# Kernel tuning notes

Hardware: AMD Instinct MI355X
Metric: run time of the kernel (lower is better)

The kernel has to match this reference:

```python
import jax, jax.numpy as jnp
import numpy as np

THETA = 10000.0

def _rope(x, pos):
    # x: [b, h, s, hd]; pos: [s]
    hd = x.shape[-1]
    inv_freq = 1.0 / (THETA ** (jnp.arange(0, hd, 2, dtype=jnp.float32) / hd))  # [hd/2]
    ang = pos.astype(jnp.float32)[:, None] * inv_freq[None, :]                   # [s, hd/2]
    cos, sin = jnp.cos(ang), jnp.sin(ang)
    x1, x2 = x[..., 0::2], x[..., 1::2]
    r1 = x1 * cos - x2 * sin
    r2 = x1 * sin + x2 * cos
    return jnp.stack([r1, r2], axis=-1).reshape(x.shape)

def setup_inputs() -> dict:
    key = jax.random.key(0)
    ks = jax.random.split(key, 5)
    b, s, d = 2, 2048, 1024
    scale = 0.02
    return {
        "x": jax.random.normal(ks[0], (b, s, d), dtype=jnp.float32),
        "Wq": jax.random.normal(ks[1], (d, d), dtype=jnp.float32) * scale,
        "Wk": jax.random.normal(ks[2], (d, d), dtype=jnp.float32) * scale,
        "Wv": jax.random.normal(ks[3], (d, d), dtype=jnp.float32) * scale,
        "Wo": jax.random.normal(ks[4], (d, d), dtype=jnp.float32) * scale,
    }

def reference(x, Wq, Wk, Wv, Wo):
    b, s, d = x.shape
    n_heads = 16
    hd = d // n_heads

    def split_heads(t):  # [b,s,d] -> [b,h,s,hd]
        return t.reshape(b, s, n_heads, hd).transpose(0, 2, 1, 3)

    q = split_heads(x @ Wq.T)
    k = split_heads(x @ Wk.T)
    v = split_heads(x @ Wv.T)

    pos = jnp.arange(s)
    q = _rope(q, pos)
    k = _rope(k, pos)

    scores = jnp.einsum("bhqd,bhkd->bhqk", q, k) / jnp.sqrt(jnp.float32(hd))
    causal = jnp.tril(jnp.ones((s, s), dtype=bool))
    scores = jnp.where(causal, scores, -jnp.inf)
    attn = jax.nn.softmax(scores, axis=-1)
    ctx = jnp.einsum("bhqk,bhkd->bhqd", attn, v)
    ctx = ctx.transpose(0, 2, 1, 3).reshape(b, s, d)
    return ctx @ Wo.T
```

## Files before the change

kernel.cpp:

```cpp
#include <hip/hip_runtime.h>
#include <math.h>

#define B  2
#define S  2048
#define D  1024
#define NH 16
#define HD 64
#define NROWS (B * S)

#define AS1 __attribute__((address_space(1)))
#define AS3 __attribute__((address_space(3)))
#define GLD16(g, l) __builtin_amdgcn_global_load_lds((const AS1 void*)(g), (AS3 void*)(l), 16, 0, 0)

typedef __attribute__((ext_vector_type(8))) short short8;
typedef __attribute__((ext_vector_type(4))) float floatx4;

#define MFMA16(a, b, c) __builtin_amdgcn_mfma_f32_16x16x32_bf16((a), (b), (c), 0, 0, 0)

__device__ inline float fexp2(float x) { return __builtin_amdgcn_exp2f(x); }

__device__ inline unsigned short f2bf(float f) {
    union { float f; unsigned int u; } v; v.f = f;
    unsigned int u = v.u;
    u += 0x7fffu + ((u >> 16) & 1);
    return (unsigned short)(u >> 16);
}

__device__ inline unsigned int pack2bf(float a, float b) {
    unsigned int ua = __float_as_uint(a) + 0x8000u;
    unsigned int ub = __float_as_uint(b) + 0x8000u;
    return __builtin_amdgcn_perm(ub, ua, 0x07060302u);
}

__global__ __launch_bounds__(256) void cvt_kernel(
    const float* __restrict__ x,  const float* __restrict__ Wq,
    const float* __restrict__ Wk, const float* __restrict__ Wv,
    const float* __restrict__ Wo,
    unsigned short* __restrict__ xb,  unsigned short* __restrict__ wqb,
    unsigned short* __restrict__ wkb, unsigned short* __restrict__ wvb,
    unsigned short* __restrict__ wob, float2* __restrict__ tab)
{
    size_t idx = (size_t)blockIdx.x * 256 + threadIdx.x;
    if (idx >= (2u << 20)) {
        int tt = (int)(idx - (2u << 20));
        int j  = tt >> 9;
        int s0 = (tt & 511) << 2;
        float invf = fexp2(-(float)j * (13.287712379549449f / 32.0f));
        #pragma unroll
        for (int p = 0; p < 4; ++p) {
            float sn, cs;
            __sincosf((float)(s0 + p) * invf, &sn, &cs);
            tab[j * 2048 + s0 + p] = make_float2(cs, sn);
        }
        return;
    }
    const float* src; unsigned short* dst; size_t off;
    if (idx < (1u << 20)) { src = x; dst = xb; off = idx << 2; }
    else {
        size_t r = idx - (1u << 20);
        int w = (int)(r >> 18);
        off = (r & ((1u << 18) - 1)) << 2;
        src = (w == 0) ? Wq : (w == 1) ? Wk : (w == 2) ? Wv : Wo;
        dst = (w == 0) ? wqb : (w == 1) ? wkb : (w == 2) ? wvb : wob;
    }
    float4 f = *(const float4*)(src + off);
    ushort4 o;
    o.x = f2bf(f.x); o.y = f2bf(f.y); o.z = f2bf(f.z); o.w = f2bf(f.w);
    *(ushort4*)(dst + off) = o;
}

#define G2STAGE(Abase, Bbase, kk, AD, BD)                                      \
{                                                                              \
    GLD16(Abase + (size_t)rowS        * D + (kk) + koS, AD + t * 8);           \
    GLD16(Abase + (size_t)(rowS + 64) * D + (kk) + koS, AD + 2048 + t * 8);    \
    GLD16(Bbase + (size_t)rowS        * D + (kk) + koS, BD + t * 8);           \
    GLD16(Bbase + (size_t)(rowS + 64) * D + (kk) + koS, BD + 2048 + t * 8);    \
}

#define G2COMP(AC, BC)                                                         \
{                                                                              \
    short8 a[4], b[4];                                                         \
    _Pragma("unroll")                                                          \
    for (int mi = 0; mi < 4; ++mi)                                             \
        a[mi] = *(const short8*)&AC[(wr * 64 + mi * 16 + lm) * 32 + quad * 8]; \
    _Pragma("unroll")                                                          \
    for (int ni = 0; ni < 4; ++ni)                                             \
        b[ni] = *(const short8*)&BC[(wc * 64 + ni * 16 + lm) * 32 + quad * 8]; \
    _Pragma("unroll")                                                          \
    for (int mi = 0; mi < 4; ++mi)                                             \
        _Pragma("unroll")                                                      \
        for (int ni = 0; ni < 4; ++ni)                                         \
            acc[mi][ni] = MFMA16(b[ni], a[mi], acc[mi][ni]);      \
}

__global__ __launch_bounds__(256, 3) void gemm_qkv_mfma(
    const unsigned short* __restrict__ xb,
    const unsigned short* __restrict__ wqb,
    const unsigned short* __restrict__ wkb,
    const unsigned short* __restrict__ wvb,
    const float2* __restrict__ tab,
    unsigned short* __restrict__ Qo, unsigned short* __restrict__ Ko,
    unsigned short* __restrict__ Vo)
{
    __shared__ short As0[128 * 32];
    __shared__ short As1[128 * 32];
    __shared__ short Bs0[128 * 32];
    __shared__ short Bs1[128 * 32];

    const int t    = threadIdx.x;
    const int wave = t >> 6, lane = t & 63;
    const int lm   = lane & 15, quad = lane >> 4;
    const int wr   = wave >> 1, wc = wave & 1;
    const int rowS = t >> 2;
    const int koS  = (t & 3) << 3;

    const int i0  = blockIdx.x * 128;
    const int by  = blockIdx.y;
    const int mat = by >> 3;
    const int j0  = (by & 7) * 128;
    const unsigned short* __restrict__ W = (mat == 0) ? wqb : (mat == 1) ? wkb : wvb;
    unsigned short* __restrict__ out = (mat == 0) ? Qo : (mat == 1) ? Ko : Vo;

    const unsigned short* Abase = xb + (size_t)i0 * D;
    const unsigned short* Bbase = W  + (size_t)j0 * D;

    floatx4 acc[4][4] = {};

    G2STAGE(Abase, Bbase, 0, As0, Bs0);
    __syncthreads();
    for (int k0 = 0; k0 < D; k0 += 64) {
        G2STAGE(Abase, Bbase, k0 + 32, As1, Bs1);
        G2COMP(As0, Bs0);
        __syncthreads();
        if (k0 + 64 < D) G2STAGE(Abase, Bbase, k0 + 64, As0, Bs0);
        G2COMP(As1, Bs1);
        __syncthreads();
    }

    const int h = (j0 + wc * 64) >> 6;
    if (mat < 2) {
        #pragma unroll
        for (int mi = 0; mi < 4; ++mi) {
            const int mg = i0 + wr * 64 + mi * 16 + lm;
            const int si = mg & (S - 1), bb = mg >> 11;
            unsigned short* orow = out + ((size_t)(bb * NH + h) * S + si) * HD;
            #pragma unroll
            for (int ni = 0; ni < 4; ++ni) {
                const int dim0 = ni * 16 + quad * 4;
                const int j = dim0 >> 1;
                float2 t0 = tab[j * 2048 + si];
                float2 t1 = tab[(j + 1) * 2048 + si];
                floatx4 v = acc[mi][ni];
                float r0 = v[0] * t0.x - v[1] * t0.y;
                float r1 = v[0] * t0.y + v[1] * t0.x;
                float r2 = v[2] * t1.x - v[3] * t1.y;
                float r3 = v[2] * t1.y + v[3] * t1.x;
                if (mat == 0) {
                    r0 *= 0.1803368801111204f; r1 *= 0.1803368801111204f;
                    r2 *= 0.1803368801111204f; r3 *= 0.1803368801111204f;
                }
                ushort4 pk;
                pk.x = f2bf(r0); pk.y = f2bf(r1);
                pk.z = f2bf(r2); pk.w = f2bf(r3);
                *(ushort4*)(orow + dim0) = pk;
            }
        }
    } else {
        #pragma unroll
        for (int mi = 0; mi < 4; ++mi) {
            const int mg = i0 + wr * 64 + mi * 16 + lm;
            const int si = mg & (S - 1), bb = mg >> 11;
            unsigned short* vb = out + (size_t)(bb * NH + h) * HD * S + si;
            #pragma unroll
            for (int ni = 0; ni < 4; ++ni) {
                const int d0 = ni * 16 + quad * 4;
                #pragma unroll
                for (int p = 0; p < 4; ++p)
                    vb[(size_t)(d0 + p) * S] = f2bf(acc[mi][ni][p]);
            }
        }
    }
}

#define GSTAGE(Abase, Bbase, kk, AD, BD)                                       \
{                                                                              \
    GLD16(Abase + (size_t)rowA  * D + (kk) + koA,  AD + cA  * 8);              \
    GLD16(Bbase + (size_t)rowB0 * D + (kk) + koB0, BD + cB0 * 8);              \
    GLD16(Bbase + (size_t)rowB1 * D + (kk) + koB1, BD + cB1 * 8);              \
}

#define GCOMP(AC, BC)                                                          \
{                                                                              \
    short8 a[4], b[2];                                                         \
    _Pragma("unroll")                                                          \
    for (int mi = 0; mi < 4; ++mi)                                             \
        a[mi] = *(const short8*)&AC[(mi * 16 + lm) * 32 + quad * 8];           \
    _Pragma("unroll")                                                          \
    for (int ni = 0; ni < 2; ++ni)                                             \
        b[ni] = *(const short8*)&BC[(wave * 32 + ni * 16 + lm) * 32 + quad * 8]; \
    _Pragma("unroll")                                                          \
    for (int mi = 0; mi < 4; ++mi)                                             \
        _Pragma("unroll")                                                      \
        for (int ni = 0; ni < 2; ++ni)                                         \
            acc[mi][ni] = MFMA16(b[ni], a[mi], acc[mi][ni]);      \
}

#define GEMM_PREAMBLE                                                          \
    const int t    = threadIdx.x;                                              \
    const int wave = t >> 6, lane = t & 63;                                    \
    const int lm   = lane & 15, quad = lane >> 4;                              \
    const int cA   = wave * 64 + lane;                                         \
    const int rowA = cA >> 2,  koA  = (cA & 3) << 3;                           \
    const int cB0  = wave * 128 + lane;                                        \
    const int rowB0 = cB0 >> 2, koB0 = (cB0 & 3) << 3;                         \
    const int cB1  = cB0 + 64;                                                 \
    const int rowB1 = cB1 >> 2, koB1 = (cB1 & 3) << 3;

#define GEMM_KLOOP(Abase, Bbase)                                               \
    GSTAGE(Abase, Bbase, 0, As0, Bs0);                                         \
    __syncthreads();                                                           \
    for (int k0 = 0; k0 < D; k0 += 64) {                                       \
        GSTAGE(Abase, Bbase, k0 + 32, As1, Bs1);                               \
        GCOMP(As0, Bs0);                                                       \
        __syncthreads();                                                       \
        if (k0 + 64 < D) GSTAGE(Abase, Bbase, k0 + 64, As0, Bs0);              \
        GCOMP(As1, Bs1);                                                       \
        __syncthreads();                                                       \
    }

__global__ __launch_bounds__(256) void gemm_out_mfma(
    const unsigned short* __restrict__ Cb,
    const unsigned short* __restrict__ wob,
    float* __restrict__ out)
{
    __shared__ short As0[64 * 32];
    __shared__ short As1[64 * 32];
    __shared__ short Bs0[128 * 32];
    __shared__ short Bs1[128 * 32];

    GEMM_PREAMBLE
    const int i0 = blockIdx.x * 64;
    const int j0 = blockIdx.y * 128;

    const unsigned short* Abase = Cb  + (size_t)i0 * D;
    const unsigned short* Bbase = wob + (size_t)j0 * D;

    floatx4 acc[4][2] = {};
    GEMM_KLOOP(Abase, Bbase)

    #pragma unroll
    for (int mi = 0; mi < 4; ++mi) {
        const int mg = i0 + mi * 16 + lm;
        float* orow = out + (size_t)mg * D;
        #pragma unroll
        for (int ni = 0; ni < 2; ++ni) {
            const int ng = j0 + wave * 32 + ni * 16 + quad * 4;
            *(floatx4*)(orow + ng) = acc[mi][ni];
        }
    }
}

__global__ __launch_bounds__(256, 4) void attn_mfma(
    const unsigned short* __restrict__ Qb,
    const unsigned short* __restrict__ Kb,
    const unsigned short* __restrict__ Vt,
    unsigned short* __restrict__ Cb)
{
    __shared__ unsigned short Ks[2][64][64];
    __shared__ unsigned short Vs[2][64][64];
    __shared__ unsigned short Ps[64][64];

    const int t    = threadIdx.x;
    const int lane = t & 63, wave = t >> 6;
    const int lm   = lane & 15, quad = lane >> 4;
    const int sw   = lm & 7;
    const int psw  = (lm & 7) << 1;

    const int b     = blockIdx.x;
    const int bh    = b & 31;
    const int f     = (b >> 5) & 7;
    const int round = b >> 8;
    int qt;
    if      (round == 0) qt = f;
    else if (round == 1) qt = 15 - f;
    else if (round == 2) qt = 16 + f;
    else                 qt = 31 - f;
    const int q0 = qt * 64;

    const unsigned short* Qg = Qb + (size_t)bh * S * HD;
    const unsigned short* Kg = Kb + (size_t)bh * S * HD;
    const unsigned short* Vg = Vt + (size_t)bh * HD * S;

    short8 qa0 = *(const short8*)(Qg + (size_t)(q0 + 16 * wave + lm) * HD + quad * 8);
    short8 qa1 = *(const short8*)(Qg + (size_t)(q0 + 16 * wave + lm) * HD + 32 + quad * 8);

    short8 vones;
    #pragma unroll
    for (int i = 0; i < 8; ++i) vones[i] = (short)0x3F80;

    #pragma unroll
    for (int i = 0; i < 2; ++i) {
        int c = t + i * 256;
        int row = c >> 3;
        int dkc = (c & 7) ^ (row & 7);
        GLD16(Kg + (size_t)row * HD + dkc * 8,        &Ks[0][0][0] + c * 8);
        GLD16(Vg + (size_t)row * S + dkc * 8,         &Vs[0][0][0] + c * 8);
        GLD16(Kg + (size_t)(64 + row) * HD + dkc * 8, &Ks[1][0][0] + c * 8);
    }

    floatx4 o[4] = {};
    floatx4 osum = {};
    floatx4 sc[4], scn[4];
    #pragma unroll
    for (int nt = 0; nt < 4; ++nt) scn[nt] = floatx4{0.f, 0.f, 0.f, 0.f};

    __syncthreads();

    #pragma unroll
    for (int nt = 0; nt < 4; ++nt) {
        short8 kb0 = *(const short8*)&Ks[0][nt * 16 + lm][(quad ^ sw) * 8];
        short8 kb1 = *(const short8*)&Ks[0][nt * 16 + lm][((4 + quad) ^ sw) * 8];
        floatx4 s = {0.f, 0.f, 0.f, 0.f};
        s = MFMA16(kb0, qa0, s);
        s = MFMA16(kb1, qa1, s);
        sc[nt] = s;
    }

    for (int kt = 0; kt <= qt; ++kt) {
        const int pb = kt & 1;

        if (kt + 2 <= qt) {
            const int k0n = (kt + 2) * 64;
            #pragma unroll
            for (int i = 0; i < 2; ++i) {
                int c = t + i * 256;
                int row = c >> 3;
                int dkc = (c & 7) ^ (row & 7);
                GLD16(Kg + (size_t)(k0n + row) * HD + dkc * 8, &Ks[pb][0][0] + c * 8);
            }
        }
        if (kt + 1 <= qt) {
            const int k0v = (kt + 1) * 64;
            #pragma unroll
            for (int i = 0; i < 2; ++i) {
                int c = t + i * 256;
                int row = c >> 3;
                int dkc = (c & 7) ^ (row & 7);
                GLD16(Vg + (size_t)row * S + k0v + dkc * 8, &Vs[pb ^ 1][0][0] + c * 8);
            }
        }

        if (kt == qt) {
            #pragma unroll
            for (int nt = 0; nt < 4; ++nt)
                #pragma unroll
                for (int r = 0; r < 4; ++r) {
                    float pe = fexp2(sc[nt][r]);
                    if (nt * 16 + quad * 4 + r > 16 * wave + lm) pe = 0.0f;
                    sc[nt][r] = pe;
                }
        } else {
            #pragma unroll
            for (int nt = 0; nt < 4; ++nt)
                #pragma unroll
                for (int r = 0; r < 4; ++r)
                    sc[nt][r] = fexp2(sc[nt][r]);
        }

        #pragma unroll
        for (int nt = 0; nt < 4; ++nt) {
            uint2 pk;
            pk.x = pack2bf(sc[nt][0], sc[nt][1]);
            pk.y = pack2bf(sc[nt][2], sc[nt][3]);
            int cp = (nt * 4 + quad) ^ psw;
            *(uint2*)&Ps[16 * wave + lm][cp * 4] = pk;
        }

        if (kt < qt) {
            #pragma unroll
            for (int nt = 0; nt < 4; ++nt) {
                short8 kb0 = *(const short8*)&Ks[pb ^ 1][nt * 16 + lm][(quad ^ sw) * 8];
                short8 kb1 = *(const short8*)&Ks[pb ^ 1][nt * 16 + lm][((4 + quad) ^ sw) * 8];
                floatx4 s = {0.f, 0.f, 0.f, 0.f};
                s = MFMA16(kb0, qa0, s);
                s = MFMA16(kb1, qa1, s);
                scn[nt] = s;
            }
        }

        short8 pa0 = *(const short8*)&Ps[16 * wave + lm][((quad * 2) ^ psw) * 4];
        short8 pa1 = *(const short8*)&Ps[16 * wave + lm][((8 + quad * 2) ^ psw) * 4];
        osum = MFMA16(pa0, vones, osum);
        osum = MFMA16(pa1, vones, osum);
        #pragma unroll
        for (int nt = 0; nt < 4; ++nt) {
            short8 vb0 = *(const short8*)&Vs[pb][nt * 16 + lm][(quad ^ sw) * 8];
            short8 vb1 = *(const short8*)&Vs[pb][nt * 16 + lm][((4 + quad) ^ sw) * 8];
            o[nt] = MFMA16(pa0, vb0, o[nt]);
            o[nt] = MFMA16(pa1, vb1, o[nt]);
        }

        __syncthreads();

        #pragma unroll
        for (int nt = 0; nt < 4; ++nt) sc[nt] = scn[nt];
    }

    const int h = bh & (NH - 1), bb = bh >> 4;
    #pragma unroll
    for (int r = 0; r < 4; ++r) {
        float inv = 1.0f / osum[r];
        size_t row = (size_t)bb * S + q0 + 16 * wave + quad * 4 + r;
        #pragma unroll
        for (int nt = 0; nt < 4; ++nt)
            Cb[row * D + h * HD + nt * 16 + lm] = f2bf(o[nt][r] * inv);
    }
}

extern "C" void kernel_launch(void* const* d_in, const int* in_sizes, int n_in,
                              void* d_out, int out_size, void* d_ws, size_t ws_size,
                              hipStream_t stream) {
    (void)in_sizes; (void)n_in; (void)out_size; (void)ws_size;
    const float* x  = (const float*)d_in[0];
    const float* Wq = (const float*)d_in[1];
    const float* Wk = (const float*)d_in[2];
    const float* Wv = (const float*)d_in[3];
    const float* Wo = (const float*)d_in[4];
    float* out = (float*)d_out;

    char* w = (char*)d_ws;
    unsigned short* Qb  = (unsigned short*)(w);
    unsigned short* Kb  = (unsigned short*)(w + (((size_t)8)  << 20));
    unsigned short* Vtb = (unsigned short*)(w + (((size_t)16) << 20));
    unsigned short* Cb  = (unsigned short*)(w + (((size_t)24) << 20));
    unsigned short* xb  = (unsigned short*)(w + (((size_t)32) << 20));
    unsigned short* wqb = (unsigned short*)(w + (((size_t)40) << 20));
    unsigned short* wkb = (unsigned short*)(w + (((size_t)42) << 20));
    unsigned short* wvb = (unsigned short*)(w + (((size_t)44) << 20));
    unsigned short* wob = (unsigned short*)(w + (((size_t)46) << 20));
    float2*         tab = (float2*)(w + (((size_t)48) << 20));

    cvt_kernel<<<8256, 256, 0, stream>>>(x, Wq, Wk, Wv, Wo,
                                         xb, wqb, wkb, wvb, wob, tab);

    dim3 g1(NROWS / 128, 24);
    gemm_qkv_mfma<<<g1, 256, 0, stream>>>(xb, wqb, wkb, wvb, tab, Qb, Kb, Vtb);

    attn_mfma<<<1024, 256, 0, stream>>>(Qb, Kb, Vtb, Cb);

    dim3 g3(NROWS / 64, D / 128);
    gemm_out_mfma<<<g3, 256, 0, stream>>>(Cb, wob, out);
}
```

Before: 168.0 us.

## Process 128-query tiles with 8 waves sharing each K/V tile load

The attention kernel now uses 512-thread blocks that each cover 128 query rows (8 waves of 16 rows), so every K/V tile staged in LDS serves twice as many queries and global K/V traffic is halved. The grid drops to 512 blocks. Each wave tracks its own causal tile count, and the upper waves do one extra tile. The lower waves sit idle through the final tile while still joining the barriers, and fewer blocks with higher LDS use may lower occupancy.

```diff
diff --git a/kernel.cpp b/kernel.cpp
--- a/kernel.cpp
+++ b/kernel.cpp
@@ -260,7 +260,7 @@
     }
 }
 
-__global__ __launch_bounds__(256, 4) void attn_mfma(
+__global__ __launch_bounds__(512, 4) void attn_mfma(
     const unsigned short* __restrict__ Qb,
     const unsigned short* __restrict__ Kb,
     const unsigned short* __restrict__ Vt,
@@ -268,7 +268,7 @@
 {
     __shared__ unsigned short Ks[2][64][64];
     __shared__ unsigned short Vs[2][64][64];
-    __shared__ unsigned short Ps[64][64];
+    __shared__ unsigned short Ps[128][64];
 
     const int t    = threadIdx.x;
     const int lane = t & 63, wave = t >> 6;
@@ -280,12 +280,10 @@
     const int bh    = b & 31;
     const int f     = (b >> 5) & 7;
     const int round = b >> 8;
-    int qt;
-    if      (round == 0) qt = f;
-    else if (round == 1) qt = 15 - f;
-    else if (round == 2) qt = 16 + f;
-    else                 qt = 31 - f;
-    const int q0 = qt * 64;
+    const int qt    = (round == 0) ? f : 15 - f;
+    const int q0    = qt * 128;
+    const int nkv   = 2 * qt + 2;
+    const int myNkv = 2 * qt + 1 + (wave >> 2);
 
     const unsigned short* Qg = Qb + (size_t)bh * S * HD;
     const unsigned short* Kg = Kb + (size_t)bh * S * HD;
@@ -298,15 +296,12 @@
     #pragma unroll
     for (int i = 0; i < 8; ++i) vones[i] = (short)0x3F80;
 
-    #pragma unroll
-    for (int i = 0; i < 2; ++i) {
-        int c = t + i * 256;
-        int row = c >> 3;
-        int dkc = (c & 7) ^ (row & 7);
-        GLD16(Kg + (size_t)row * HD + dkc * 8,        &Ks[0][0][0] + c * 8);
-        GLD16(Vg + (size_t)row * S + dkc * 8,         &Vs[0][0][0] + c * 8);
-        GLD16(Kg + (size_t)(64 + row) * HD + dkc * 8, &Ks[1][0][0] + c * 8);
-    }
+    const int srow = t >> 3;
+    const int sch  = (t & 7) ^ (srow & 7);
+
+    GLD16(Kg + (size_t)srow * HD + sch * 8,        &Ks[0][0][0] + t * 8);
+    GLD16(Vg + (size_t)srow * S + sch * 8,         &Vs[0][0][0] + t * 8);
+    GLD16(Kg + (size_t)(64 + srow) * HD + sch * 8, &Ks[1][0][0] + t * 8);
 
     floatx4 o[4] = {};
     floatx4 osum = {};
@@ -326,84 +321,77 @@
         sc[nt] = s;
     }
 
-    for (int kt = 0; kt <= qt; ++kt) {
+    __syncthreads();
+
+    for (int kt = 0; kt < nkv; ++kt) {
         const int pb = kt & 1;
 
-        if (kt + 2 <= qt) {
-            const int k0n = (kt + 2) * 64;
-            #pragma unroll
-            for (int i = 0; i < 2; ++i) {
-                int c = t + i * 256;
-                int row = c >> 3;
-                int dkc = (c & 7) ^ (row & 7);
-                GLD16(Kg + (size_t)(k0n + row) * HD + dkc * 8, &Ks[pb][0][0] + c * 8);
-            }
-        }
-        if (kt + 1 <= qt) {
-            const int k0v = (kt + 1) * 64;
-            #pragma unroll
-            for (int i = 0; i < 2; ++i) {
-                int c = t + i * 256;
-                int row = c >> 3;
-                int dkc = (c & 7) ^ (row & 7);
-                GLD16(Vg + (size_t)row * S + k0v + dkc * 8, &Vs[pb ^ 1][0][0] + c * 8);
-            }
-        }
-
-        if (kt == qt) {
-            #pragma unroll
-            for (int nt = 0; nt < 4; ++nt)
+        if (kt + 2 < nkv)
+            GLD16(Kg + (size_t)((kt + 2) * 64 + srow) * HD + sch * 8,
+                  &Ks[pb][0][0] + t * 8);
+        if (kt + 1 < nkv)
+            GLD16(Vg + (size_t)srow * S + (kt + 1) * 64 + sch * 8,
+                  &Vs[pb ^ 1][0][0] + t * 8);
+
+        if (kt < myNkv) {
+            if (kt == myNkv - 1) {
+                const int rel = q0 + 16 * wave + lm - kt * 64;
                 #pragma unroll
-                for (int r = 0; r < 4; ++r) {
-                    float pe = fexp2(sc[nt][r]);
-                    if (nt * 16 + quad * 4 + r > 16 * wave + lm) pe = 0.0f;
-                    sc[nt][r] = pe;
-                }
-        } else {
-            #pragma unroll
-            for (int nt = 0; nt < 4; ++nt)
+                for (int nt = 0; nt < 4; ++nt)
+                    #pragma unroll
+                    for (int r = 0; r < 4; ++r) {
+                        float pe = fexp2(sc[nt][r]);
+                        if (nt * 16 + quad * 4 + r > rel) pe = 0.0f;
+                        sc[nt][r] = pe;
+                    }
+            } else {
                 #pragma unroll
-                for (int r = 0; r < 4; ++r)
-                    sc[nt][r] = fexp2(sc[nt][r]);
-        }
-
-        #pragma unroll
-        for (int nt = 0; nt < 4; ++nt) {
-            uint2 pk;
-            pk.x = pack2bf(sc[nt][0], sc[nt][1]);
-            pk.y = pack2bf(sc[nt][2], sc[nt][3]);
-            int cp = (nt * 4 + quad) ^ psw;
-            *(uint2*)&Ps[16 * wave + lm][cp * 4] = pk;
-        }
-
-        if (kt < qt) {
+                for (int nt = 0; nt < 4; ++nt)
+                    #pragma unroll
+                    for (int r = 0; r < 4; ++r)
+                        sc[nt][r] = fexp2(sc[nt][r]);
+            }
+
             #pragma unroll
             for (int nt = 0; nt < 4; ++nt) {
-                short8 kb0 = *(const short8*)&Ks[pb ^ 1][nt * 16 + lm][(quad ^ sw) * 8];
-                short8 kb1 = *(const short8*)&Ks[pb ^ 1][nt * 16 + lm][((4 + quad) ^ sw) * 8];
-                floatx4 s = {0.f, 0.f, 0.f, 0.f};
-                s = MFMA16(kb0, qa0, s);
-                s = MFMA16(kb1, qa1, s);
-                scn[nt] = s;
-            }
-        }
-
-        short8 pa0 = *(const short8*)&Ps[16 * wave + lm][((quad * 2) ^ psw) * 4];
-        short8 pa1 = *(const short8*)&Ps[16 * wave + lm][((8 + quad * 2) ^ psw) * 4];
-        osum = MFMA16(pa0, vones, osum);
-        osum = MFMA16(pa1, vones, osum);
-        #pragma unroll
-        for (int nt = 0; nt < 4; ++nt) {
-            short8 vb0 = *(const short8*)&Vs[pb][nt * 16 + lm][(quad ^ sw) * 8];
-            short8 vb1 = *(const short8*)&Vs[pb][nt * 16 + lm][((4 + quad) ^ sw) * 8];
-            o[nt] = MFMA16(pa0, vb0, o[nt]);
-            o[nt] = MFMA16(pa1, vb1, o[nt]);
+                uint2 pk;
+                pk.x = pack2bf(sc[nt][0], sc[nt][1]);
+                pk.y = pack2bf(sc[nt][2], sc[nt][3]);
+                int cp = (nt * 4 + quad) ^ psw;
+                *(uint2*)&Ps[16 * wave + lm][cp * 4] = pk;
+            }
+
+            if (kt + 1 < myNkv) {
+                #pragma unroll
+                for (int nt = 0; nt < 4; ++nt) {
+                    short8 kb0 = *(const short8*)&Ks[pb ^ 1][nt * 16 + lm][(quad ^ sw) * 8];
+                    short8 kb1 = *(const short8*)&Ks[pb ^ 1][nt * 16 + lm][((4 + quad) ^ sw) * 8];
+                    floatx4 s = {0.f, 0.f, 0.f, 0.f};
+                    s = MFMA16(kb0, qa0, s);
+                    s = MFMA16(kb1, qa1, s);
+                    scn[nt] = s;
+                }
+            }
+
+            short8 pa0 = *(const short8*)&Ps[16 * wave + lm][((quad * 2) ^ psw) * 4];
+            short8 pa1 = *(const short8*)&Ps[16 * wave + lm][((8 + quad * 2) ^ psw) * 4];
+            osum = MFMA16(pa0, vones, osum);
+            osum = MFMA16(pa1, vones, osum);
+            #pragma unroll
+            for (int nt = 0; nt < 4; ++nt) {
+                short8 vb0 = *(const short8*)&Vs[pb][nt * 16 + lm][(quad ^ sw) * 8];
+                short8 vb1 = *(const short8*)&Vs[pb][nt * 16 + lm][((4 + quad) ^ sw) * 8];
+                o[nt] = MFMA16(pa0, vb0, o[nt]);
+                o[nt] = MFMA16(pa1, vb1, o[nt]);
+            }
         }
 
         __syncthreads();
 
-        #pragma unroll
-        for (int nt = 0; nt < 4; ++nt) sc[nt] = scn[nt];
+        if (kt + 1 < myNkv) {
+            #pragma unroll
+            for (int nt = 0; nt < 4; ++nt) sc[nt] = scn[nt];
+        }
     }
 
     const int h = bh & (NH - 1), bb = bh >> 4;
@@ -446,7 +434,7 @@
     dim3 g1(NROWS / 128, 24);
     gemm_qkv_mfma<<<g1, 256, 0, stream>>>(xb, wqb, wkb, wvb, tab, Qb, Kb, Vtb);
 
-    attn_mfma<<<1024, 256, 0, stream>>>(Qb, Kb, Vtb, Cb);
+    attn_mfma<<<512, 512, 0, stream>>>(Qb, Kb, Vtb, Cb);
 
     dim3 g3(NROWS / 64, D / 128);
     gemm_out_mfma<<<g3, 256, 0, stream>>>(Cb, wob, out);
```

Measured after the change: 168.3 us (median of 2 runs). About the same (+0.2%).

## Split long causal attention rows across two KV chunks with a combine pass

Applied to the files above, without the earlier changes.

Query tiles 16-31 are split into two KV-range chunks processed by separate blocks, so the causal workload is balanced across 1536 blocks under a constant-memory schedule that issues the longest tiles first. Partial unnormalized outputs and row sums go to a float workspace, and a new combine kernel adds the two chunks and normalizes. No max subtraction is used, so partials can be summed directly. MFMA sections are also raised in wave priority with s_setprio. The cost is an extra launch and a round trip of partials through global memory.

```diff
diff --git a/kernel.cpp b/kernel.cpp
--- a/kernel.cpp
+++ b/kernel.cpp
@@ -260,11 +260,17 @@
     }
 }
 
+__constant__ unsigned char attn_sched[48] = {
+    32,34,36,38,40,42,44,46,48,50,52,54,56,58,60,62,30,63,
+    28,61, 26,59, 24,57, 22,55, 20,53, 18,51, 16,49, 14,47,
+    12,45, 10,43,  8,41,  6,39,  4,37,  2,35,  0,33 };
+
 __global__ __launch_bounds__(256, 4) void attn_mfma(
     const unsigned short* __restrict__ Qb,
     const unsigned short* __restrict__ Kb,
     const unsigned short* __restrict__ Vt,
-    unsigned short* __restrict__ Cb)
+    unsigned short* __restrict__ Cb,
+    float* __restrict__ Pb)
 {
     __shared__ unsigned short Ks[2][64][64];
     __shared__ unsigned short Vs[2][64][64];
@@ -276,16 +282,16 @@
     const int sw   = lm & 7;
     const int psw  = (lm & 7) << 1;
 
-    const int b     = blockIdx.x;
-    const int bh    = b & 31;
-    const int f     = (b >> 5) & 7;
-    const int round = b >> 8;
-    int qt;
-    if      (round == 0) qt = f;
-    else if (round == 1) qt = 15 - f;
-    else if (round == 2) qt = 16 + f;
-    else                 qt = 31 - f;
-    const int q0 = qt * 64;
+    const int bid   = blockIdx.x;
+    const int bh    = bid & 31;
+    const int slot  = bid >> 5;
+    const int e     = attn_sched[slot];
+    const int qt    = e >> 1;
+    const int chunk = e & 1;
+    const int k_lo  = chunk << 4;
+    const int khi0  = (chunk + 1) << 4;
+    const int k_hi  = (khi0 < qt + 1) ? khi0 : qt + 1;
+    const int q0    = qt * 64;
 
     const unsigned short* Qg = Qb + (size_t)bh * S * HD;
     const unsigned short* Kg = Kb + (size_t)bh * S * HD;
@@ -303,9 +309,9 @@
         int c = t + i * 256;
         int row = c >> 3;
         int dkc = (c & 7) ^ (row & 7);
-        GLD16(Kg + (size_t)row * HD + dkc * 8,        &Ks[0][0][0] + c * 8);
-        GLD16(Vg + (size_t)row * S + dkc * 8,         &Vs[0][0][0] + c * 8);
-        GLD16(Kg + (size_t)(64 + row) * HD + dkc * 8, &Ks[1][0][0] + c * 8);
+        GLD16(Kg + (size_t)(k_lo * 64 + row) * HD + dkc * 8,       &Ks[0][0][0] + c * 8);
+        GLD16(Vg + (size_t)row * S + k_lo * 64 + dkc * 8,          &Vs[0][0][0] + c * 8);
+        GLD16(Kg + (size_t)((k_lo + 1) * 64 + row) * HD + dkc * 8, &Ks[1][0][0] + c * 8);
     }
 
     floatx4 o[4] = {};
@@ -326,27 +332,29 @@
         sc[nt] = s;
     }
 
-    for (int kt = 0; kt <= qt; ++kt) {
-        const int pb = kt & 1;
-
-        if (kt + 2 <= qt) {
-            const int k0n = (kt + 2) * 64;
+    __syncthreads();
+
+    for (int kt = k_lo; kt < k_hi; ++kt) {
+        const int pb = (kt - k_lo) & 1;
+
+        if (kt + 2 < k_hi) {
             #pragma unroll
             for (int i = 0; i < 2; ++i) {
                 int c = t + i * 256;
                 int row = c >> 3;
                 int dkc = (c & 7) ^ (row & 7);
-                GLD16(Kg + (size_t)(k0n + row) * HD + dkc * 8, &Ks[pb][0][0] + c * 8);
+                GLD16(Kg + (size_t)((kt + 2) * 64 + row) * HD + dkc * 8,
+                      &Ks[pb][0][0] + c * 8);
             }
         }
-        if (kt + 1 <= qt) {
-            const int k0v = (kt + 1) * 64;
+        if (kt + 1 < k_hi) {
             #pragma unroll
             for (int i = 0; i < 2; ++i) {
                 int c = t + i * 256;
                 int row = c >> 3;
                 int dkc = (c & 7) ^ (row & 7);
-                GLD16(Vg + (size_t)row * S + k0v + dkc * 8, &Vs[pb ^ 1][0][0] + c * 8);
+                GLD16(Vg + (size_t)row * S + (kt + 1) * 64 + dkc * 8,
+                      &Vs[pb ^ 1][0][0] + c * 8);
             }
         }
 
@@ -376,7 +384,7 @@
             *(uint2*)&Ps[16 * wave + lm][cp * 4] = pk;
         }
 
-        if (kt < qt) {
+        if (kt + 1 < k_hi) {
             #pragma unroll
             for (int nt = 0; nt < 4; ++nt) {
                 short8 kb0 = *(const short8*)&Ks[pb ^ 1][nt * 16 + lm][(quad ^ sw) * 8];
@@ -390,6 +398,7 @@
 
         short8 pa0 = *(const short8*)&Ps[16 * wave + lm][((quad * 2) ^ psw) * 4];
         short8 pa1 = *(const short8*)&Ps[16 * wave + lm][((8 + quad * 2) ^ psw) * 4];
+        __builtin_amdgcn_s_setprio(1);
         osum = MFMA16(pa0, vones, osum);
         osum = MFMA16(pa1, vones, osum);
         #pragma unroll
@@ -399,6 +408,7 @@
             o[nt] = MFMA16(pa0, vb0, o[nt]);
             o[nt] = MFMA16(pa1, vb1, o[nt]);
         }
+        __builtin_amdgcn_s_setprio(0);
 
         __syncthreads();
 
@@ -406,15 +416,45 @@
         for (int nt = 0; nt < 4; ++nt) sc[nt] = scn[nt];
     }
 
+    if (qt < 16) {
+        const int h = bh & (NH - 1), bb = bh >> 4;
+        #pragma unroll
+        for (int r = 0; r < 4; ++r) {
+            float inv = 1.0f / osum[r];
+            size_t row = (size_t)bb * S + q0 + 16 * wave + quad * 4 + r;
+            #pragma unroll
+            for (int nt = 0; nt < 4; ++nt)
+                Cb[row * D + h * HD + nt * 16 + lm] = f2bf(o[nt][r] * inv);
+        }
+    } else {
+        float* pbuf = Pb + (size_t)((((bh << 4) + (qt - 16)) << 1) + chunk) * 4224;
+        #pragma unroll
+        for (int r = 0; r < 4; ++r) {
+            const int q = 16 * wave + quad * 4 + r;
+            #pragma unroll
+            for (int nt = 0; nt < 4; ++nt)
+                pbuf[q * 64 + nt * 16 + lm] = o[nt][r];
+            if (lm == 0) pbuf[4096 + q] = osum[r];
+        }
+    }
+}
+
+__global__ __launch_bounds__(256) void attn_combine(
+    const float* __restrict__ Pb, unsigned short* __restrict__ Cb)
+{
+    const int tile = blockIdx.x;
+    const int bh = tile & 31, qi = tile >> 5;
+    const float* p0 = Pb + (size_t)(((bh << 4) + qi) << 1) * 4224;
+    const float* p1 = p0 + 4224;
+    const int t = threadIdx.x;
+    const int q = t >> 2, dg = (t & 3) << 4;
+    const float inv = 1.0f / (p0[4096 + q] + p1[4096 + q]);
     const int h = bh & (NH - 1), bb = bh >> 4;
-    #pragma unroll
-    for (int r = 0; r < 4; ++r) {
-        float inv = 1.0f / osum[r];
-        size_t row = (size_t)bb * S + q0 + 16 * wave + quad * 4 + r;
-        #pragma unroll
-        for (int nt = 0; nt < 4; ++nt)
-            Cb[row * D + h * HD + nt * 16 + lm] = f2bf(o[nt][r] * inv);
-    }
+    const size_t row = (size_t)bb * S + (size_t)(16 + qi) * 64 + q;
+    unsigned short* dst = Cb + row * D + h * HD + dg;
+    #pragma unroll
+    for (int j = 0; j < 16; ++j)
+        dst[j] = f2bf((p0[q * 64 + dg + j] + p1[q * 64 + dg + j]) * inv);
 }
 
 extern "C" void kernel_launch(void* const* d_in, const int* in_sizes, int n_in,
@@ -439,6 +479,7 @@
     unsigned short* wvb = (unsigned short*)(w + (((size_t)44) << 20));
     unsigned short* wob = (unsigned short*)(w + (((size_t)46) << 20));
     float2*         tab = (float2*)(w + (((size_t)48) << 20));
+    float*          Pb  = (float*)(w + (((size_t)64) << 20));
 
     cvt_kernel<<<8256, 256, 0, stream>>>(x, Wq, Wk, Wv, Wo,
                                          xb, wqb, wkb, wvb, wob, tab);
@@ -446,7 +487,8 @@
     dim3 g1(NROWS / 128, 24);
     gemm_qkv_mfma<<<g1, 256, 0, stream>>>(xb, wqb, wkb, wvb, tab, Qb, Kb, Vtb);
 
-    attn_mfma<<<1024, 256, 0, stream>>>(Qb, Kb, Vtb, Cb);
+    attn_mfma<<<1536, 256, 0, stream>>>(Qb, Kb, Vtb, Cb, Pb);
+    attn_combine<<<512, 256, 0, stream>>>(Pb, Cb);
 
     dim3 g3(NROWS / 64, D / 128);
     gemm_out_mfma<<<g3, 256, 0, stream>>>(Cb, wob, out);
```

New measurement: 169.0 us. About the same (+0.6%).
